# Kernel tuning notes

Hardware: AMD Instinct MI355X
Metric: run time of the kernel (lower is better)

The kernel has to match this reference:

```python
import jax, jax.numpy as jnp
import numpy as np

B, N, D, H, NCTX = 4, 2048, 1024, 16, 512
HD = D // H  # head dim = 64


def setup_inputs() -> dict:
    key = jax.random.key(0)
    ks = jax.random.split(key, 6)
    return {
        "x": jax.random.normal(ks[0], (B, N, D), dtype=jnp.float32),
        "ctx_ppr": jax.random.uniform(ks[1], (B, NCTX), dtype=jnp.float32),
        "ctx_trust": jax.random.normal(ks[2], (B, NCTX), dtype=jnp.float32),
        "W_in": jax.random.normal(ks[3], (D, 3 * D), dtype=jnp.float32) * 0.02,
        "b_in": jnp.zeros((3 * D,), dtype=jnp.float32),
        "W_out": jax.random.normal(ks[4], (D, D), dtype=jnp.float32) * 0.02,
        "b_out": jnp.zeros((D,), dtype=jnp.float32),
        "log_ppr_alpha": jnp.full((1,), 0.1, dtype=jnp.float32),
        "trust_scale": jnp.full((1,), 0.1, dtype=jnp.float32),
        "n_ctx": NCTX,
    }


def reference(x, ctx_ppr, ctx_trust, W_in, b_in, W_out, b_out, log_ppr_alpha, trust_scale, n_ctx):
    b, n, dmodel = x.shape
    # QKV projection
    qkv = x @ W_in + b_in                                   # [B,N,3D]
    q, k, v = jnp.split(qkv, 3, axis=-1)
    q = q.reshape(b, n, H, HD).transpose(0, 2, 1, 3)        # [B,H,N,d]
    k = k.reshape(b, n, H, HD).transpose(0, 2, 1, 3)
    v = v.reshape(b, n, H, HD).transpose(0, 2, 1, 3)
    if n_ctx > 0:
        # multiplicative trust gate on context-token values
        gate = jax.nn.sigmoid(trust_scale * ctx_trust)      # [B,n_ctx]
        gate_full = jnp.concatenate(
            [gate, jnp.ones((b, n - n_ctx), dtype=x.dtype)], axis=1)  # [B,N]
        v = v * gate_full[:, None, :, None]
        # additive graph (log-PPR) column bias on attention logits
        col_bias = -log_ppr_alpha * jnp.log(jnp.maximum(ctx_ppr, 1e-8))  # [B,n_ctx]
        bias = jnp.concatenate(
            [col_bias, jnp.zeros((b, n - n_ctx), dtype=x.dtype)], axis=1)  # [B,N]
    else:
        bias = jnp.zeros((b, n), dtype=x.dtype)
    scale = 1.0 / np.sqrt(HD).astype(np.float32)
    scores = jnp.einsum("bhqd,bhkd->bhqk", q, k) * scale + bias[:, None, None, :]
    attn = jax.nn.softmax(scores, axis=-1)                  # [B,H,N,N]
    out = jnp.einsum("bhqk,bhkd->bhqd", attn, v)            # [B,H,N,d]
    out = out.transpose(0, 2, 1, 3).reshape(b, n, dmodel)
    return out @ W_out + b_out
```

## Files before the change

kernel.cpp:

```cpp
#include <hip/hip_runtime.h>
#include <hip/hip_bf16.h>
#include <stdint.h>

#define BATCH  4
#define NSEQ   2048
#define DMODEL 1024
#define NHEAD  16
#define HDIM   64
#define NCTXC  512

typedef unsigned short u16;
typedef __attribute__((ext_vector_type(8))) short bfrag;
typedef __attribute__((ext_vector_type(4))) float facc;

typedef __attribute__((address_space(3))) void lds_void;
typedef __attribute__((address_space(1))) void g_void;

__device__ __forceinline__ void gload16(const void* g, void* l) {
  __builtin_amdgcn_global_load_lds((const g_void*)g, (lds_void*)l, 16, 0, 0);
}

__device__ __forceinline__ u16 f2bf(float f) {
  uint32_t r;
  asm("v_cvt_pk_bf16_f32 %0, %1, %1" : "=v"(r) : "v"(f));
  return (u16)r;
}

#if __has_builtin(__builtin_amdgcn_cvt_pk_bf16_f32)
__device__ __forceinline__ uint32_t pk2bf(float a, float b) {
  return __builtin_bit_cast(uint32_t, __builtin_amdgcn_cvt_pk_bf16_f32(a, b));
}
#else
__device__ __forceinline__ uint32_t pk2bf(float a, float b) {
  uint32_t r;
  asm("v_cvt_pk_bf16_f32 %0, %1, %2" : "=v"(r) : "v"(a), "v"(b));
  return r;
}
#endif

__device__ __forceinline__ float bf2f(u16 h) {
  union { uint32_t u; float f; } un;
  un.u = ((uint32_t)h) << 16;
  return un.f;
}

__device__ __forceinline__ float load_flex(const void* p, size_t idx, int isb) {
  return isb ? bf2f(((const u16*)p)[idx]) : ((const float*)p)[idx];
}

__device__ __forceinline__ uint4 pack8(float4 a, float4 b) {
  uint4 r;
  r.x = pk2bf(a.x, a.y);
  r.y = pk2bf(a.z, a.w);
  r.z = pk2bf(b.x, b.y);
  r.w = pk2bf(b.z, b.w);
  return r;
}

__global__ __launch_bounds__(256) void detect_kernel(const u16* __restrict__ xraw,
                                                     int* __restrict__ flag) {
  __shared__ int s_high, s_zero;
  if (threadIdx.x == 0) { s_high = 0; s_zero = 0; }
  __syncthreads();
  int h = 0, z = 0;
  for (int i = threadIdx.x; i < 4096; i += 256) {
    const u16 v = xraw[2 * i];
    const int e = (v >> 7) & 0xFF;
    if (e >= 0x90) h++;
    if (v == 0) z++;
  }
  atomicAdd(&s_high, h);
  atomicAdd(&s_zero, z);
  __syncthreads();
  if (threadIdx.x == 0) flag[0] = (s_high < 64 && s_zero < 2048) ? 1 : 0;
}


__global__ __launch_bounds__(256) void cast_x_kernel(const void* __restrict__ x,
                                                     u16* __restrict__ xb,
                                                     const int* __restrict__ flag) {
  const int isb = flag[0];
  const int i = blockIdx.x * 256 + threadIdx.x;
  if (isb) {
    ((uint4*)xb)[i] = ((const uint4*)x)[i];
  } else {
    const float4 f0 = ((const float4*)x)[2 * i];
    const float4 f1 = ((const float4*)x)[2 * i + 1];
    ((uint4*)xb)[i] = pack8(f0, f1);
  }
}

__global__ __launch_bounds__(256) void transpose_flex(const void* __restrict__ W,
                                                      u16* __restrict__ Wt,
                                                      int R, int C,
                                                      const int* __restrict__ flag) {
  __shared__ float tile[32][33];
  const int isb = flag[0];
  const int tx = threadIdx.x;
  const int ty = threadIdx.y;
  const int c0 = blockIdx.x * 32;
  const int r0 = blockIdx.y * 32;
#pragma unroll
  for (int j = 0; j < 32; j += 8)
    tile[ty + j][tx] = load_flex(W, (size_t)(r0 + ty + j) * C + c0 + tx, isb);
  __syncthreads();
#pragma unroll
  for (int j = 0; j < 32; j += 8)
    Wt[(size_t)(c0 + ty + j) * R + r0 + tx] = f2bf(tile[tx][ty + j]);
}

__global__ __launch_bounds__(256) void prep_small(const void* __restrict__ b_in,
                                                  const void* __restrict__ b_out,
                                                  const void* __restrict__ ppr,
                                                  const void* __restrict__ trust,
                                                  const void* __restrict__ alpha_p,
                                                  const void* __restrict__ ts_p,
                                                  float* __restrict__ bin_f,
                                                  float* __restrict__ bout_f,
                                                  float* __restrict__ gate,
                                                  float* __restrict__ cbias,
                                                  const int* __restrict__ flag) {
  const int isb = flag[0];
  const int i = blockIdx.x * 256 + threadIdx.x;
  if (i < 3072) {
    bin_f[i] = load_flex(b_in, i, isb);
  } else if (i < 4096) {
    bout_f[i - 3072] = load_flex(b_out, i - 3072, isb);
  } else if (i < 4096 + BATCH * NCTXC) {
    const int j = i - 4096;
    const float ts = load_flex(ts_p, 0, isb), al = load_flex(alpha_p, 0, isb);
    gate[j]  = 1.0f / (1.0f + __expf(-ts * load_flex(trust, j, isb)));
    cbias[j] = -al * logf(fmaxf(load_flex(ppr, j, isb), 1e-8f)) * 1.44269504f;
  }
}

__device__ __forceinline__ void kloop_mfma(const u16* __restrict__ Ag,
                                           const u16* __restrict__ Bg,
                                           u16* As, u16* Bs,
                                           int tid, int wM, int wN, int l16, int quad,
                                           facc acc[4][4]) {
  char* ldsA = (char*)As + tid * 16;
  char* ldsB = (char*)Bs + tid * 16;
  for (int k0 = 0; k0 < 1024; k0 += 32) {
    __syncthreads();
    gload16(Ag + k0, ldsA);
    gload16(Ag + (size_t)64 * 1024 + k0, ldsA + 4096);
    gload16(Bg + k0, ldsB);
    gload16(Bg + (size_t)64 * 1024 + k0, ldsB + 4096);
    __syncthreads();

    bfrag af[4], bf[4];
#pragma unroll
    for (int i = 0; i < 4; ++i)
      af[i] = *(const bfrag*)(&As[(wM + i * 16 + l16) * 32 + quad * 8]);
#pragma unroll
    for (int j = 0; j < 4; ++j)
      bf[j] = *(const bfrag*)(&Bs[(wN + j * 16 + l16) * 32 + quad * 8]);
#pragma unroll
    for (int i = 0; i < 4; ++i)
#pragma unroll
      for (int j = 0; j < 4; ++j)
        acc[i][j] = __builtin_amdgcn_mfma_f32_16x16x32_bf16(af[i], bf[j], acc[i][j], 0, 0, 0);
  }
}

__global__ __launch_bounds__(256) void gemm_qkvt(const u16* __restrict__ xb,
                                                 const u16* __restrict__ Wt,
                                                 const float* __restrict__ bin_f,
                                                 const float* __restrict__ gate,
                                                 u16* __restrict__ qk,
                                                 u16* __restrict__ Vtg) {
  __shared__ u16 As[128 * 32];
  __shared__ u16 Bs[128 * 32];
  const int tid  = threadIdx.x;
  const int w    = tid >> 6;
  const int lane = tid & 63;
  const int quad = lane >> 4;
  const int l16  = lane & 15;
  const int wM   = (w >> 1) * 64;
  const int wN   = (w & 1) * 64;
  const int id   = blockIdx.x;
  const int srow  = tid >> 2;
  const int spart = tid & 3;

  facc acc[4][4] = {};

  if (id < 1024) {
    const int bn = id & 15, bm = id >> 4;
    const u16* Ag = xb + (size_t)(bm * 128 + srow) * 1024 + spart * 8;
    const u16* Bg = Wt + (size_t)(bn * 128 + srow) * 1024 + spart * 8;
    kloop_mfma(Ag, Bg, As, Bs, tid, wM, wN, l16, quad, acc);

    const float qs = (bn < 8) ? 0.18033688f : 1.0f;
#pragma unroll
    for (int i = 0; i < 4; ++i) {
      const int grow0 = bm * 128 + wM + i * 16 + quad * 4;
#pragma unroll
      for (int j = 0; j < 4; ++j) {
        const int gcol = bn * 128 + wN + j * 16 + l16;
        const float bv = bin_f[gcol];
#pragma unroll
        for (int r = 0; r < 4; ++r)
          qk[(size_t)(grow0 + r) * 2048 + gcol] = f2bf((acc[i][j][r] + bv) * qs);
      }
    }
  } else {
    const int id2 = id - 1024;
    const int bn = id2 & 63, bm = id2 >> 6;
    const u16* Ag = Wt + (size_t)2048 * 1024 + (size_t)(bm * 128 + srow) * 1024 + spart * 8;
    const u16* Bg = xb + (size_t)(bn * 128 + srow) * 1024 + spart * 8;
    kloop_mfma(Ag, Bg, As, Bs, tid, wM, wN, l16, quad, acc);

#pragma unroll
    for (int i = 0; i < 4; ++i) {
      const int grow0 = bm * 128 + wM + i * 16 + quad * 4;
      const int h   = grow0 >> 6;
      const int dd0 = grow0 & 63;
#pragma unroll
      for (int j = 0; j < 4; ++j) {
        const int gcol = bn * 128 + wN + j * 16 + l16;
        const int bb  = gcol >> 11;
        const int tok = gcol & (NSEQ - 1);
        const float gl = (tok < NCTXC) ? gate[bb * NCTXC + tok] : 1.0f;
        u16* dst = &Vtg[((size_t)((bb * NHEAD + h) * HDIM + dd0)) * NSEQ + tok];
#pragma unroll
        for (int r = 0; r < 4; ++r)
          dst[(size_t)r * NSEQ] = f2bf((acc[i][j][r] + bin_f[2 * DMODEL + grow0 + r]) * gl);
      }
    }
  }
}

__global__ __launch_bounds__(256) void gemm_out(const u16* __restrict__ A,
                                                const u16* __restrict__ Bt,
                                                const float* __restrict__ biasf,
                                                void* __restrict__ Cout,
                                                const int* __restrict__ flag) {
  __shared__ u16 As[128 * 32];
  __shared__ u16 Bs[128 * 32];
  const int isb  = flag[0];
  const int tid  = threadIdx.x;
  const int w    = tid >> 6;
  const int lane = tid & 63;
  const int quad = lane >> 4;
  const int l16  = lane & 15;
  const int wM   = (w >> 1) * 64;
  const int wN   = (w & 1) * 64;
  const int bm   = blockIdx.y;
  const int bn   = blockIdx.x;
  const int srow  = tid >> 2;
  const int spart = tid & 3;

  facc acc[4][4] = {};
  const u16* Ag = A + (size_t)(bm * 128 + srow) * 2048 + spart * 8;
  const u16* Bg = Bt + (size_t)(bn * 128 + srow) * 1024 + spart * 8;
  char* ldsA = (char*)As + tid * 16;
  char* ldsB = (char*)Bs + tid * 16;

  for (int k0 = 0; k0 < 1024; k0 += 32) {
    __syncthreads();
    gload16(Ag + k0, ldsA);
    gload16(Ag + (size_t)64 * 2048 + k0, ldsA + 4096);
    gload16(Bg + k0, ldsB);
    gload16(Bg + (size_t)64 * 1024 + k0, ldsB + 4096);
    __syncthreads();

    bfrag af[4], bf[4];
#pragma unroll
    for (int i = 0; i < 4; ++i)
      af[i] = *(const bfrag*)(&As[(wM + i * 16 + l16) * 32 + quad * 8]);
#pragma unroll
    for (int j = 0; j < 4; ++j)
      bf[j] = *(const bfrag*)(&Bs[(wN + j * 16 + l16) * 32 + quad * 8]);
#pragma unroll
    for (int i = 0; i < 4; ++i)
#pragma unroll
      for (int j = 0; j < 4; ++j)
        acc[i][j] = __builtin_amdgcn_mfma_f32_16x16x32_bf16(af[i], bf[j], acc[i][j], 0, 0, 0);
  }

#pragma unroll
  for (int i = 0; i < 4; ++i) {
    const int grow0 = bm * 128 + wM + i * 16 + quad * 4;
#pragma unroll
    for (int j = 0; j < 4; ++j) {
      const int gcol = bn * 128 + wN + j * 16 + l16;
      const float bv = biasf[gcol];
#pragma unroll
      for (int r = 0; r < 4; ++r) {
        const float v = acc[i][j][r] + bv;
        if (isb) ((u16*)Cout)[(size_t)(grow0 + r) * 1024 + gcol] = f2bf(v);
        else     ((float*)Cout)[(size_t)(grow0 + r) * 1024 + gcol] = v;
      }
    }
  }
}

__global__ __launch_bounds__(256) void attn_kernel(u16* __restrict__ qk,
                                                   const u16* __restrict__ vtg,
                                                   const float* __restrict__ cbias) {
  const int id    = blockIdx.x;
  const int chunk = id >> 3;
  const int qt    = chunk & 15;
  const int hg    = (id & 7) | ((chunk >> 4) << 3);
  const int h     = hg & 15;
  const int b     = hg >> 4;

  __shared__ u16 Ks[64 * 72];
  __shared__ u16 Vt[64 * 72];

  const int tid  = threadIdx.x;
  const int w    = tid >> 6;
  const int lane = tid & 63;
  const int quad = lane >> 4;
  const int l16  = lane & 15;
  const int srow = tid >> 2;
  const int spart = tid & 3;

  bfrag bq[2][2];
#pragma unroll
  for (int qs = 0; qs < 2; ++qs) {
    const u16* qrow = qk + (size_t)(b * NSEQ + qt * 128 + (w * 2 + qs) * 16 + l16) * 2048 + h * HDIM;
    bq[qs][0] = *(const bfrag*)(qrow + quad * 8);
    bq[qs][1] = *(const bfrag*)(qrow + 32 + quad * 8);
  }

  bfrag ones;
#pragma unroll
  for (int i = 0; i < 8; ++i) ones[i] = (short)0x3F80;

  facc den[2] = {};
  facc o[2][4] = {};

  const u16* kst = qk + (size_t)(b * NSEQ) * 2048 + DMODEL + h * HDIM;
  const u16* vst = vtg + (size_t)((b * NHEAD + h) * HDIM + srow) * NSEQ;

  uint4 pk0, pk1, pv0, pv1;
  {
    const u16* ks = kst + (size_t)srow * 2048 + spart * 16;
    pk0 = *(const uint4*)ks;
    pk1 = *(const uint4*)(ks + 8);
    const u16* vs = vst + spart * 16;
    pv0 = *(const uint4*)vs;
    pv1 = *(const uint4*)(vs + 8);
  }

  for (int t = 0; t < NSEQ / 64; ++t) {
    __syncthreads();
    *(uint4*)(&Ks[srow * 72 + spart * 16])     = pk0;
    *(uint4*)(&Ks[srow * 72 + spart * 16 + 8]) = pk1;
    *(uint4*)(&Vt[srow * 72 + spart * 16])     = pv0;
    *(uint4*)(&Vt[srow * 72 + spart * 16 + 8]) = pv1;
    __syncthreads();

    {
      const int tn = (t < NSEQ / 64 - 1) ? t + 1 : t;
      const u16* ks = kst + (size_t)(tn * 64 + srow) * 2048 + spart * 16;
      pk0 = *(const uint4*)ks;
      pk1 = *(const uint4*)(ks + 8);
      const u16* vs = vst + tn * 64 + spart * 16;
      pv0 = *(const uint4*)vs;
      pv1 = *(const uint4*)(vs + 8);
    }

    bfrag ak[4][2];
#pragma unroll
    for (int nt = 0; nt < 4; ++nt) {
      ak[nt][0] = *(const bfrag*)(&Ks[(nt * 16 + l16) * 72 + quad * 8]);
      ak[nt][1] = *(const bfrag*)(&Ks[(nt * 16 + l16) * 72 + 32 + quad * 8]);
    }

    bfrag av[4][2];
#pragma unroll
    for (int dt = 0; dt < 4; ++dt) {
      const u16* vr = &Vt[(dt * 16 + l16) * 72];
#pragma unroll
      for (int half = 0; half < 2; ++half) {
        union { bfrag f; uint2 u2[2]; } un;
        un.u2[0] = *(const uint2*)(vr + half * 32 + quad * 4);
        un.u2[1] = *(const uint2*)(vr + half * 32 + 16 + quad * 4);
        av[dt][half] = un.f;
      }
    }

    facc zb[4];
    if (t < 8) {
      const float* cb = cbias + b * NCTXC + t * 64 + quad * 4;
#pragma unroll
      for (int nt = 0; nt < 4; ++nt) zb[nt] = *(const facc*)(cb + nt * 16);
    } else {
#pragma unroll
      for (int nt = 0; nt < 4; ++nt) zb[nt] = (facc){};
    }

#pragma unroll
    for (int qs = 0; qs < 2; ++qs) {
      facc s[4];
      __builtin_amdgcn_s_setprio(1);
#pragma unroll
      for (int nt = 0; nt < 4; ++nt) {
        facc z = zb[nt];
        z = __builtin_amdgcn_mfma_f32_16x16x32_bf16(ak[nt][0], bq[qs][0], z, 0, 0, 0);
        s[nt] = __builtin_amdgcn_mfma_f32_16x16x32_bf16(ak[nt][1], bq[qs][1], z, 0, 0, 0);
      }
      __builtin_amdgcn_s_setprio(0);

#pragma unroll
      for (int nt = 0; nt < 4; ++nt)
#pragma unroll
        for (int r = 0; r < 4; ++r)
          s[nt][r] = __builtin_amdgcn_exp2f(s[nt][r]);

      union { bfrag f; uint32_t wrd[4]; } bp0, bp1;
      bp0.wrd[0] = pk2bf(s[0][0], s[0][1]);
      bp0.wrd[1] = pk2bf(s[0][2], s[0][3]);
      bp0.wrd[2] = pk2bf(s[1][0], s[1][1]);
      bp0.wrd[3] = pk2bf(s[1][2], s[1][3]);
      bp1.wrd[0] = pk2bf(s[2][0], s[2][1]);
      bp1.wrd[1] = pk2bf(s[2][2], s[2][3]);
      bp1.wrd[2] = pk2bf(s[3][0], s[3][1]);
      bp1.wrd[3] = pk2bf(s[3][2], s[3][3]);

      __builtin_amdgcn_s_setprio(1);
#pragma unroll
      for (int dt = 0; dt < 4; ++dt) {
        o[qs][dt] = __builtin_amdgcn_mfma_f32_16x16x32_bf16(av[dt][0], bp0.f, o[qs][dt], 0, 0, 0);
        o[qs][dt] = __builtin_amdgcn_mfma_f32_16x16x32_bf16(av[dt][1], bp1.f, o[qs][dt], 0, 0, 0);
      }
      den[qs] = __builtin_amdgcn_mfma_f32_16x16x32_bf16(ones, bp0.f, den[qs], 0, 0, 0);
      den[qs] = __builtin_amdgcn_mfma_f32_16x16x32_bf16(ones, bp1.f, den[qs], 0, 0, 0);
      __builtin_amdgcn_s_setprio(0);
    }
  }

#pragma unroll
  for (int qs = 0; qs < 2; ++qs) {
    const float inv = 1.0f / den[qs][0];
    u16* orow = qk + (size_t)(b * NSEQ + qt * 128 + (w * 2 + qs) * 16 + l16) * 2048 + h * HDIM;
#pragma unroll
    for (int dt = 0; dt < 4; ++dt) {
      uint2 st;
      st.x = pk2bf(o[qs][dt][0] * inv, o[qs][dt][1] * inv);
      st.y = pk2bf(o[qs][dt][2] * inv, o[qs][dt][3] * inv);
      *(uint2*)(orow + dt * 16 + quad * 4) = st;
    }
  }
}


extern "C" void kernel_launch(void* const* d_in, const int* in_sizes, int n_in,
                              void* d_out, int out_size, void* d_ws, size_t ws_size,
                              hipStream_t stream) {
  const void* x          = d_in[0];
  const void* ctx_ppr    = d_in[1];
  const void* ctx_trust  = d_in[2];
  const void* W_in       = d_in[3];
  const void* b_in       = d_in[4];
  const void* W_out      = d_in[5];
  const void* b_out      = d_in[6];
  const void* lppr_alpha = d_in[7];
  const void* tscale     = d_in[8];

  char* ws = (char*)d_ws;
  u16* Wt    = (u16*)ws;  ws += (size_t)3072 * 1024 * 2;
  u16* WoT   = (u16*)ws;  ws += (size_t)1024 * 1024 * 2;
  u16* qk    = (u16*)ws;  ws += (size_t)8192 * 2048 * 2;
  u16* Vtg   = (u16*)ws;  ws += (size_t)64 * 64 * 2048 * 2;
  u16* xb    = (u16*)ws;  ws += (size_t)8192 * 1024 * 2;
  float* bin_f  = (float*)ws; ws += 3072 * 4;
  float* bout_f = (float*)ws; ws += 1024 * 4;
  float* gate   = (float*)ws; ws += (size_t)BATCH * NCTXC * 4;
  float* cbias  = (float*)ws; ws += (size_t)BATCH * NCTXC * 4;
  int*   flag   = (int*)ws;   ws += 64;

  detect_kernel<<<dim3(1), dim3(256), 0, stream>>>((const u16*)x, flag);
  cast_x_kernel<<<dim3(4096), dim3(256), 0, stream>>>(x, xb, flag);
  transpose_flex<<<dim3(96, 32), dim3(32, 8), 0, stream>>>(W_in, Wt, 1024, 3072, flag);
  transpose_flex<<<dim3(32, 32), dim3(32, 8), 0, stream>>>(W_out, WoT, 1024, 1024, flag);
  prep_small<<<dim3(24), dim3(256), 0, stream>>>(b_in, b_out, ctx_ppr, ctx_trust,
                                                 lppr_alpha, tscale,
                                                 bin_f, bout_f, gate, cbias, flag);
  gemm_qkvt<<<dim3(1536), dim3(256), 0, stream>>>(xb, Wt, bin_f, gate, qk, Vtg);
  attn_kernel<<<dim3(1024), dim3(256), 0, stream>>>(qk, Vtg, cbias);
  gemm_out<<<dim3(8, 64), dim3(256), 0, stream>>>(qk, WoT, bout_f, d_out, flag);
}
```

Baseline: 301.1 us.

## Restructure attention kernel with async LDS double buffering and fewer waves

```diff
diff --git a/kernel.cpp b/kernel.cpp
--- a/kernel.cpp
+++ b/kernel.cpp
@@ -296,9 +296,9 @@
   }
 }
 
-__global__ __launch_bounds__(256) void attn_kernel(u16* __restrict__ qk,
-                                                   const u16* __restrict__ vtg,
-                                                   const float* __restrict__ cbias) {
+__global__ __launch_bounds__(128, 2) void attn_kernel(u16* __restrict__ qk,
+                                                      const u16* __restrict__ vtg,
+                                                      const float* __restrict__ cbias) {
   const int id    = blockIdx.x;
   const int chunk = id >> 3;
   const int qt    = chunk & 15;
@@ -306,21 +306,18 @@
   const int h     = hg & 15;
   const int b     = hg >> 4;
 
-  __shared__ u16 Ks[64 * 72];
-  __shared__ u16 Vt[64 * 72];
+  __shared__ u16 KV[2][2][64 * 64];
 
   const int tid  = threadIdx.x;
   const int w    = tid >> 6;
   const int lane = tid & 63;
   const int quad = lane >> 4;
   const int l16  = lane & 15;
-  const int srow = tid >> 2;
-  const int spart = tid & 3;
-
-  bfrag bq[2][2];
-#pragma unroll
-  for (int qs = 0; qs < 2; ++qs) {
-    const u16* qrow = qk + (size_t)(b * NSEQ + qt * 128 + (w * 2 + qs) * 16 + l16) * 2048 + h * HDIM;
+
+  bfrag bq[4][2];
+#pragma unroll
+  for (int qs = 0; qs < 4; ++qs) {
+    const u16* qrow = qk + (size_t)(b * NSEQ + qt * 128 + w * 64 + qs * 16 + l16) * 2048 + h * HDIM;
     bq[qs][0] = *(const bfrag*)(qrow + quad * 8);
     bq[qs][1] = *(const bfrag*)(qrow + 32 + quad * 8);
   }
@@ -329,58 +326,61 @@
 #pragma unroll
   for (int i = 0; i < 8; ++i) ones[i] = (short)0x3F80;
 
-  facc den[2] = {};
-  facc o[2][4] = {};
-
-  const u16* kst = qk + (size_t)(b * NSEQ) * 2048 + DMODEL + h * HDIM;
-  const u16* vst = vtg + (size_t)((b * NHEAD + h) * HDIM + srow) * NSEQ;
-
-  uint4 pk0, pk1, pv0, pv1;
-  {
-    const u16* ks = kst + (size_t)srow * 2048 + spart * 16;
-    pk0 = *(const uint4*)ks;
-    pk1 = *(const uint4*)(ks + 8);
-    const u16* vs = vst + spart * 16;
-    pv0 = *(const uint4*)vs;
-    pv1 = *(const uint4*)(vs + 8);
-  }
+  facc den[4] = {};
+  facc o[4][4] = {};
+
+  const u16* kbase = qk + (size_t)(b * NSEQ) * 2048 + DMODEL + h * HDIM;
+  const u16* vbase = vtg + (size_t)((b * NHEAD + h) * HDIM) * NSEQ;
+
+  int crow[4], csc[4];
+#pragma unroll
+  for (int i = 0; i < 4; ++i) {
+    const int c = tid + i * 128;
+    crow[i] = c >> 3;
+    csc[i]  = (c & 7) ^ (crow[i] & 7);
+  }
+
+  const int e    = l16 & 7;
+  const int swk0 = (quad ^ e) * 8;
+  const int cA0  = ((quad >> 1) ^ e) * 8 + (quad & 1) * 4;
+
+  auto stage = [&](int sel, int t) {
+#pragma unroll
+    for (int i = 0; i < 4; ++i) {
+      const int c = tid + i * 128;
+      gload16(kbase + (size_t)(t * 64 + crow[i]) * 2048 + csc[i] * 8, &KV[sel][0][c * 8]);
+      gload16(vbase + (size_t)crow[i] * 2048 + t * 64 + csc[i] * 8,   &KV[sel][1][c * 8]);
+    }
+  };
+
+  stage(0, 0);
 
   for (int t = 0; t < NSEQ / 64; ++t) {
     __syncthreads();
-    *(uint4*)(&Ks[srow * 72 + spart * 16])     = pk0;
-    *(uint4*)(&Ks[srow * 72 + spart * 16 + 8]) = pk1;
-    *(uint4*)(&Vt[srow * 72 + spart * 16])     = pv0;
-    *(uint4*)(&Vt[srow * 72 + spart * 16 + 8]) = pv1;
-    __syncthreads();
-
-    {
-      const int tn = (t < NSEQ / 64 - 1) ? t + 1 : t;
-      const u16* ks = kst + (size_t)(tn * 64 + srow) * 2048 + spart * 16;
-      pk0 = *(const uint4*)ks;
-      pk1 = *(const uint4*)(ks + 8);
-      const u16* vs = vst + tn * 64 + spart * 16;
-      pv0 = *(const uint4*)vs;
-      pv1 = *(const uint4*)(vs + 8);
-    }
+    if (t + 1 < NSEQ / 64) stage((t + 1) & 1, t + 1);
+
+    const u16* Kb = KV[t & 1][0];
+    const u16* Vb = KV[t & 1][1];
 
     bfrag ak[4][2];
 #pragma unroll
     for (int nt = 0; nt < 4; ++nt) {
-      ak[nt][0] = *(const bfrag*)(&Ks[(nt * 16 + l16) * 72 + quad * 8]);
-      ak[nt][1] = *(const bfrag*)(&Ks[(nt * 16 + l16) * 72 + 32 + quad * 8]);
+      const u16* kr = &Kb[(nt * 16 + l16) * 64];
+      ak[nt][0] = *(const bfrag*)(kr + swk0);
+      ak[nt][1] = *(const bfrag*)(kr + (swk0 ^ 32));
     }
 
     bfrag av[4][2];
 #pragma unroll
     for (int dt = 0; dt < 4; ++dt) {
-      const u16* vr = &Vt[(dt * 16 + l16) * 72];
-#pragma unroll
-      for (int half = 0; half < 2; ++half) {
-        union { bfrag f; uint2 u2[2]; } un;
-        un.u2[0] = *(const uint2*)(vr + half * 32 + quad * 4);
-        un.u2[1] = *(const uint2*)(vr + half * 32 + 16 + quad * 4);
-        av[dt][half] = un.f;
-      }
+      const u16* vr = &Vb[(dt * 16 + l16) * 64];
+      union { bfrag f; uint2 u2[2]; } un0, un1;
+      un0.u2[0] = *(const uint2*)(vr + cA0);
+      un0.u2[1] = *(const uint2*)(vr + (cA0 ^ 16));
+      un1.u2[0] = *(const uint2*)(vr + (cA0 ^ 32));
+      un1.u2[1] = *(const uint2*)(vr + (cA0 ^ 48));
+      av[dt][0] = un0.f;
+      av[dt][1] = un1.f;
     }
 
     facc zb[4];
@@ -394,7 +394,7 @@
     }
 
 #pragma unroll
-    for (int qs = 0; qs < 2; ++qs) {
+    for (int qs = 0; qs < 4; ++qs) {
       facc s[4];
       __builtin_amdgcn_s_setprio(1);
 #pragma unroll
@@ -434,9 +434,9 @@
   }
 
 #pragma unroll
-  for (int qs = 0; qs < 2; ++qs) {
+  for (int qs = 0; qs < 4; ++qs) {
     const float inv = 1.0f / den[qs][0];
-    u16* orow = qk + (size_t)(b * NSEQ + qt * 128 + (w * 2 + qs) * 16 + l16) * 2048 + h * HDIM;
+    u16* orow = qk + (size_t)(b * NSEQ + qt * 128 + w * 64 + qs * 16 + l16) * 2048 + h * HDIM;
 #pragma unroll
     for (int dt = 0; dt < 4; ++dt) {
       uint2 st;
@@ -481,6 +481,6 @@
                                                  lppr_alpha, tscale,
                                                  bin_f, bout_f, gate, cbias, flag);
   gemm_qkvt<<<dim3(1536), dim3(256), 0, stream>>>(xb, Wt, bin_f, gate, qk, Vtg);
-  attn_kernel<<<dim3(1024), dim3(256), 0, stream>>>(qk, Vtg, cbias);
+  attn_kernel<<<dim3(1024), dim3(128), 0, stream>>>(qk, Vtg, cbias);
   gemm_out<<<dim3(8, 64), dim3(256), 0, stream>>>(qk, WoT, bout_f, d_out, flag);
 }
```

Result: faster. 285.7 us (-5.1%).
